# Kernel optimization log

Measured on AMD Instinct MI355X. Metric: run time of the kernel, lower is better.

Reference implementation:

```python
import jax, jax.numpy as jnp
import numpy as np

ITER_NUM = 3
BN_EPS = 1e-5
L2_EPS = 1e-12


def setup_inputs() -> dict:
    key = jax.random.key(0)
    k1, k2 = jax.random.split(key, 2)
    B, C, h, w = 64, 256, 14, 14
    E = 512
    feat = jax.random.normal(k1, (B, C, h, w), dtype=jnp.float32)
    W_proj = jax.random.normal(k2, (E, C * C), dtype=jnp.float32) * (1.0 / np.sqrt(C * C))
    b_proj = jnp.zeros((E,), dtype=jnp.float32)
    bn_gamma = jnp.ones((E,), dtype=jnp.float32)
    bn_beta = jnp.zeros((E,), dtype=jnp.float32)
    bn_mean = jnp.zeros((E,), dtype=jnp.float32)
    bn_var = jnp.ones((E,), dtype=jnp.float32)
    return {"feat": feat, "W_proj": W_proj, "b_proj": b_proj,
            "bn_gamma": bn_gamma, "bn_beta": bn_beta,
            "bn_mean": bn_mean, "bn_var": bn_var}


def _mpncov(feat):
    # feat: [B, C, h, w] -> [B, C, C] matrix square root of normalized covariance
    B, C, h, w = feat.shape
    M = h * w
    x = feat.reshape(B, C, M)
    # I_hat = I - (1/M) * ones  (centering matrix)
    I_hat = jnp.eye(M, dtype=feat.dtype) - (1.0 / M) * jnp.ones((M, M), dtype=feat.dtype)
    # y = x @ I_hat @ x^T / M  -> [B, C, C]
    xc = jnp.einsum('bcm,mn->bcn', x, I_hat)
    y = jnp.einsum('bcm,bdm->bcd', xc, x) / M
    trY = jnp.trace(y, axis1=-2, axis2=-1)  # [B]
    y = y / trY[:, None, None]
    I = jnp.broadcast_to(jnp.eye(C, dtype=feat.dtype), (B, C, C))
    Y, Z = y, I
    for _ in range(ITER_NUM):
        ZY = jnp.einsum('bij,bjk->bik', Z, Y)
        T = 3.0 * I - ZY
        Y = 0.5 * jnp.einsum('bij,bjk->bik', Y, T)
        Z = 0.5 * jnp.einsum('bij,bjk->bik', T, Z)
    return Y * jnp.sqrt(trY)[:, None, None]


def _l2_normalize(x, axis=-1):
    n = jnp.sqrt(jnp.sum(x * x, axis=axis, keepdims=True))
    return x / jnp.maximum(n, L2_EPS)


def reference(feat, W_proj, b_proj, bn_gamma, bn_beta, bn_mean, bn_var):
    B = feat.shape[0]
    pooled = _mpncov(feat)                      # [B, C, C]
    flat = pooled.reshape(B, -1)                # [B, C*C]
    flat = _l2_normalize(flat, axis=1)
    # dropout in eval mode = identity
    emb = flat @ W_proj.T + b_proj              # [B, E]
    # BatchNorm1d (inference mode, running stats)
    emb = (emb - bn_mean) * jax.lax.rsqrt(bn_var + BN_EPS) * bn_gamma + bn_beta
    norm_embedding = _l2_normalize(emb, axis=1)
    return norm_embedding
```

## Files before the change

### kernel.cpp

```cpp
#include <hip/hip_runtime.h>
#include <hip/hip_bf16.h>

#define BATCH 64
#define CDIM  256
#define MHW   196
#define MP    224
#define EDIM  512
#define CC    65536
#define NTRI  10

typedef __attribute__((ext_vector_type(8))) short short8_t;
typedef __attribute__((ext_vector_type(4))) float f32x4;
typedef __attribute__((ext_vector_type(4))) unsigned int u32x4;

static __device__ __forceinline__ short f2bf(float f) {
    __hip_bfloat16 h = __float2bfloat16(f);
    return (short)__builtin_bit_cast(unsigned short, h);
}

struct MMOp {
    const __hip_bfloat16* A;
    const __hip_bfloat16* B;
    const __hip_bfloat16* D;
    __hip_bfloat16*       out;
    const float*          alpha_ptr;
    int                   alpha_mode;
    float                 alpha_c, beta, gamma;
    float*                nrm;
};

__global__ __launch_bounds__(256) void k_center(const float* __restrict__ feat,
                                                __hip_bfloat16* __restrict__ xcb,
                                                float* __restrict__ rowsq)
{
    const int row = blockIdx.x * 4 + (threadIdx.x >> 6);
    const int l = threadIdx.x & 63;
    const float* src = feat + (size_t)row * MHW;
    float v0 = src[l];
    float v1 = src[l + 64];
    float v2 = src[l + 128];
    float v3 = (l + 192 < MHW) ? src[l + 192] : 0.0f;
    float s = v0 + v1 + v2 + v3;
    #pragma unroll
    for (int o = 32; o >= 1; o >>= 1) s += __shfl_xor(s, o, 64);
    const float mean = s * (1.0f / MHW);
    v0 -= mean; v1 -= mean; v2 -= mean;
    v3 = (l + 192 < MHW) ? (v3 - mean) : 0.0f;
    float sq = v0*v0 + v1*v1 + v2*v2 + v3*v3;
    #pragma unroll
    for (int o = 32; o >= 1; o >>= 1) sq += __shfl_xor(sq, o, 64);
    if (l == 0) rowsq[row] = sq;
    __hip_bfloat16* dst = xcb + (size_t)row * MP;
    dst[l]       = __float2bfloat16(v0);
    dst[l + 64]  = __float2bfloat16(v1);
    dst[l + 128] = __float2bfloat16(v2);
    if (l + 192 < MP) dst[l + 192] = __float2bfloat16(v3);
}

template<int KT, bool NORM>
__global__ __launch_bounds__(256) void k_mm(MMOp op0, MMOp op1)
{
    const MMOp& op = (blockIdx.y == 0) ? op0 : op1;

    __shared__ __hip_bfloat16 As[64][72];
    __shared__ __hip_bfloat16 Bs[64][72];
    __shared__ float red[4];
    __shared__ float s_alpha;

    const int b = blockIdx.x / NTRI;
    const int t = blockIdx.x - b * NTRI;
    int ti, tj;
    if (t < 4)      { ti = 0; tj = t; }
    else if (t < 7) { ti = 1; tj = t - 3; }
    else if (t < 9) { ti = 2; tj = t - 5; }
    else            { ti = 3; tj = 3; }

    const int tid = threadIdx.x;
    const int wv = tid >> 6, l = tid & 63;
    const int wr = wv >> 1, wc = wv & 1;
    const int lr = l & 15,  lg = l >> 4;

    if (op.alpha_mode) {
        float v = op.alpha_ptr[b * 256 + tid];
        #pragma unroll
        for (int o = 32; o >= 1; o >>= 1) v += __shfl_xor(v, o, 64);
        if (l == 0) red[wv] = v;
        __syncthreads();
        if (tid == 0) s_alpha = op.alpha_c / (red[0] + red[1] + red[2] + red[3]);
    } else if (tid == 0) {
        s_alpha = op.alpha_c;
    }

    const __hip_bfloat16* Ab = op.A + (size_t)b * (CDIM * KT) + (size_t)ti * 64 * KT;
    const __hip_bfloat16* Bb = op.B + (size_t)b * (CDIM * KT) + (size_t)tj * 64 * KT;

    f32x4 acc[2][2];
    #pragma unroll
    for (int i = 0; i < 2; i++)
        #pragma unroll
        for (int j = 0; j < 2; j++)
            #pragma unroll
            for (int r = 0; r < 4; r++) acc[i][j][r] = 0.0f;

    #pragma unroll
    for (int k0 = 0; k0 < KT; k0 += 64) {
        const int kw   = (KT - k0 >= 64) ? 64 : (KT - k0);
        const int segs = kw >> 3;
        __syncthreads();
        for (int u = tid; u < 64 * segs; u += 256) {
            const int row = u / segs;
            const int seg = u - row * segs;
            *reinterpret_cast<u32x4*>(&As[row][seg * 8]) =
                *reinterpret_cast<const u32x4*>(Ab + (size_t)row * KT + k0 + seg * 8);
            *reinterpret_cast<u32x4*>(&Bs[row][seg * 8]) =
                *reinterpret_cast<const u32x4*>(Bb + (size_t)row * KT + k0 + seg * 8);
        }
        __syncthreads();
        const int nks = kw >> 5;
        for (int ks = 0; ks < nks; ks++) {
            short8_t af[2], bfr[2];
            #pragma unroll
            for (int i = 0; i < 2; i++)
                af[i] = *reinterpret_cast<const short8_t*>(&As[wr * 32 + i * 16 + lr][ks * 32 + lg * 8]);
            #pragma unroll
            for (int j = 0; j < 2; j++)
                bfr[j] = *reinterpret_cast<const short8_t*>(&Bs[wc * 32 + j * 16 + lr][ks * 32 + lg * 8]);
            #pragma unroll
            for (int i = 0; i < 2; i++)
                #pragma unroll
                for (int j = 0; j < 2; j++)
                    acc[i][j] = __builtin_amdgcn_mfma_f32_16x16x32_bf16(af[i], bfr[j], acc[i][j], 0, 0, 0);
        }
    }

    const float a = s_alpha;
    __hip_bfloat16* ob = op.out + (size_t)b * CC;
    const __hip_bfloat16* Db = op.D ? (op.D + (size_t)b * CC) : nullptr;
    float ns = 0.0f;
    #pragma unroll
    for (int i = 0; i < 2; i++) {
        #pragma unroll
        for (int j = 0; j < 2; j++) {
            #pragma unroll
            for (int r = 0; r < 4; r++) {
                const int grow = ti * 64 + wr * 32 + i * 16 + lg * 4 + r;
                const int gcol = tj * 64 + wc * 32 + j * 16 + lr;
                float v = a * acc[i][j][r];
                if (Db) v += op.beta * __bfloat162float(Db[grow * 256 + gcol]);
                if (grow == gcol) v += op.gamma;
                const __hip_bfloat16 hv = __float2bfloat16(v);
                ob[grow * 256 + gcol] = hv;
                if (ti != tj) ob[gcol * 256 + grow] = hv;
                if (NORM) {
                    const float fv = __bfloat162float(hv);
                    ns += ((ti != tj) ? 2.0f : 1.0f) * fv * fv;
                }
            }
        }
    }
    if constexpr (NORM) {
        #pragma unroll
        for (int o = 32; o >= 1; o >>= 1) ns += __shfl_xor(ns, o, 64);
        __syncthreads();
        if (l == 0) red[wv] = ns;
        __syncthreads();
        if (tid == 0) op.nrm[b * NTRI + t] = red[0] + red[1] + red[2] + red[3];
    }
}

__global__ __launch_bounds__(256) void k_proj(const __hip_bfloat16* __restrict__ flat,
                                              const float* __restrict__ W,
                                              float* __restrict__ upart)
{
    const int ks = blockIdx.x;
    const int et = blockIdx.y;
    const int tid = threadIdx.x, wv = tid >> 6, l = tid & 63;
    const int lr = l & 15, lg = l >> 4;
    const int kbase = ks * 2048 + wv * 512;

    f32x4 acc[4][4];
    #pragma unroll
    for (int i = 0; i < 4; i++)
        #pragma unroll
        for (int j = 0; j < 4; j++)
            #pragma unroll
            for (int r = 0; r < 4; r++) acc[i][j][r] = 0.0f;

    for (int kk = 0; kk < 512; kk += 32) {
        const int k = kbase + kk + lg * 8;
        short8_t af[4];
        #pragma unroll
        for (int i = 0; i < 4; i++)
            af[i] = *reinterpret_cast<const short8_t*>(flat + (size_t)(i * 16 + lr) * CC + k);
        short8_t bfr[4];
        #pragma unroll
        for (int j = 0; j < 4; j++) {
            const f32x4* wp = reinterpret_cast<const f32x4*>(W + (size_t)(et * 64 + j * 16 + lr) * CC + k);
            const f32x4 w0 = wp[0], w1 = wp[1];
            short8_t s;
            s[0] = f2bf(w0[0]); s[1] = f2bf(w0[1]); s[2] = f2bf(w0[2]); s[3] = f2bf(w0[3]);
            s[4] = f2bf(w1[0]); s[5] = f2bf(w1[1]); s[6] = f2bf(w1[2]); s[7] = f2bf(w1[3]);
            bfr[j] = s;
        }
        #pragma unroll
        for (int i = 0; i < 4; i++)
            #pragma unroll
            for (int j = 0; j < 4; j++)
                acc[i][j] = __builtin_amdgcn_mfma_f32_16x16x32_bf16(af[i], bfr[j], acc[i][j], 0, 0, 0);
    }

    __shared__ float racc[2][64][65];
    if (wv >= 2) {
        #pragma unroll
        for (int i = 0; i < 4; i++)
            #pragma unroll
            for (int j = 0; j < 4; j++)
                #pragma unroll
                for (int r = 0; r < 4; r++)
                    racc[wv - 2][i * 16 + lg * 4 + r][j * 16 + lr] = acc[i][j][r];
    }
    __syncthreads();
    if (wv < 2) {
        #pragma unroll
        for (int i = 0; i < 4; i++)
            #pragma unroll
            for (int j = 0; j < 4; j++)
                #pragma unroll
                for (int r = 0; r < 4; r++)
                    racc[wv][i * 16 + lg * 4 + r][j * 16 + lr] += acc[i][j][r];
    }
    __syncthreads();
    float* ub = upart + (size_t)ks * (64 * EDIM);
    #pragma unroll
    for (int q = 0; q < 16; q++) {
        const int idx = q * 256 + tid;
        const int x = idx >> 6, y = idx & 63;
        ub[(size_t)x * EDIM + et * 64 + y] = racc[0][x][y] + racc[1][x][y];
    }
}

__global__ __launch_bounds__(512) void k_final(const float* __restrict__ upart,
                                               const float* __restrict__ nrmp,
                                               const float* __restrict__ bias,
                                               const float* __restrict__ gma,
                                               const float* __restrict__ bta,
                                               const float* __restrict__ mu,
                                               const float* __restrict__ var,
                                               float* __restrict__ out)
{
    const int b = blockIdx.x;
    const int e = threadIdx.x;
    float u = 0.0f;
    for (int p = 0; p < 32; p++)
        u += upart[((size_t)p * 64 + b) * EDIM + e];
    float fro = 0.0f;
    #pragma unroll
    for (int q = 0; q < NTRI; q++) fro += nrmp[b * NTRI + q];
    const float s = 1.0f / fmaxf(sqrtf(fro), 1e-12f);
    const float emb = s * u + bias[e];
    const float v = (emb - mu[e]) * rsqrtf(var[e] + 1e-5f) * gma[e] + bta[e];
    float sq = v * v;
    #pragma unroll
    for (int o = 32; o >= 1; o >>= 1) sq += __shfl_xor(sq, o, 64);
    __shared__ float wsum[8];
    if ((e & 63) == 0) wsum[e >> 6] = sq;
    __syncthreads();
    float tot = 0.0f;
    #pragma unroll
    for (int i = 0; i < 8; i++) tot += wsum[i];
    out[(size_t)b * EDIM + e] = v / fmaxf(sqrtf(tot), 1e-12f);
}

extern "C" void kernel_launch(void* const* d_in, const int* in_sizes, int n_in,
                              void* d_out, int out_size, void* d_ws, size_t ws_size,
                              hipStream_t stream)
{
    const float* feat = (const float*)d_in[0];
    const float* W    = (const float*)d_in[1];
    const float* bias = (const float*)d_in[2];
    const float* gma  = (const float*)d_in[3];
    const float* bta  = (const float*)d_in[4];
    const float* mu   = (const float*)d_in[5];
    const float* var  = (const float*)d_in[6];
    float* out = (float*)d_out;

    char* ws = (char*)d_ws;
    constexpr size_t XCB_BYTES = (size_t)BATCH * CDIM * MP * 2;
    constexpr size_t MATB      = (size_t)BATCH * CC * 2;
    constexpr size_t OFF_ROWSQ = 4096;
    constexpr size_t OFF_XCB   = OFF_ROWSQ + (size_t)BATCH * CDIM * 4;
    constexpr size_t OFF_M     = OFF_XCB + XCB_BYTES;
    constexpr size_t OFF_UP    = OFF_M + 5 * MATB;
    constexpr size_t NEEDED    = OFF_UP + (size_t)32 * 64 * EDIM * 4;
    if (ws_size < NEEDED) return;

    float* nrmp  = (float*)(ws + 1024);
    float* rowsq = (float*)(ws + OFF_ROWSQ);
    __hip_bfloat16* xcb = (__hip_bfloat16*)(ws + OFF_XCB);
    __hip_bfloat16* M0  = (__hip_bfloat16*)(ws + OFF_M + 0 * MATB);
    __hip_bfloat16* M1  = (__hip_bfloat16*)(ws + OFF_M + 1 * MATB);
    __hip_bfloat16* M2  = (__hip_bfloat16*)(ws + OFF_M + 2 * MATB);
    __hip_bfloat16* M3  = (__hip_bfloat16*)(ws + OFF_M + 3 * MATB);
    __hip_bfloat16* M4  = (__hip_bfloat16*)(ws + OFF_M + 4 * MATB);
    float* upart = (float*)(ws + OFF_UP);

    k_center<<<dim3(4096), dim3(256), 0, stream>>>(feat, xcb, rowsq);

    const dim3 g1(BATCH * NTRI, 1), g2(BATCH * NTRI, 2), blk(256);
    MMOp nop = {};

    MMOp cov = {xcb, xcb, nullptr, M0, rowsq, 1, 1.0f, 0.0f, 0.0f, nullptr};
    k_mm<MP, false><<<g1, blk, 0, stream>>>(cov, nop);
    MMOp y1 = {M0, M0, M0, M1, nullptr, 0, -0.5f, 1.5f, 0.0f, nullptr};
    k_mm<256, false><<<g1, blk, 0, stream>>>(y1, nop);
    MMOp t2 = {M0, M1, M1, M2, nullptr, 0, 0.5f, -1.5f, 3.0f, nullptr};
    k_mm<256, false><<<g1, blk, 0, stream>>>(t2, nop);
    MMOp y2 = {M1, M2, nullptr, M3, nullptr, 0, 0.5f, 0.0f, 0.0f, nullptr};
    MMOp z2 = {M2, M0, M2, M4, nullptr, 0, -0.25f, 0.75f, 0.0f, nullptr};
    k_mm<256, false><<<g2, blk, 0, stream>>>(y2, z2);
    MMOp t3 = {M4, M3, nullptr, M1, nullptr, 0, -1.0f, 0.0f, 3.0f, nullptr};
    k_mm<256, false><<<g1, blk, 0, stream>>>(t3, nop);
    MMOp y3 = {M3, M1, nullptr, M2, nullptr, 0, 0.5f, 0.0f, 0.0f, nrmp};
    k_mm<256, true ><<<g1, blk, 0, stream>>>(y3, nop);

    k_proj<<<dim3(32, 8), blk, 0, stream>>>(M2, W, upart);
    k_final<<<dim3(64), 512, 0, stream>>>(upart, nrmp, bias, gma, bta, mu, var, out);
}
```

Baseline: 133.1 us.

## Fuse Newton-Schulz chain into cooperative persistent kernel with grid syncs

Replaces the sequence of centering and batched matmul launches with one cooperative kernel that uses grid-wide syncs between stages. The projection and final normalization are fused into a second cooperative kernel. The projection K-split is doubled to give 512 blocks. This targets per-launch overhead and tail gaps between small dependent kernels. In exchange it adds grid.sync costs and host-side occupancy queries on every call, and it keeps a multi-launch fallback path.

```diff
diff --git a/kernel.cpp b/kernel.cpp
--- a/kernel.cpp
+++ b/kernel.cpp
@@ -1,5 +1,8 @@
 #include <hip/hip_runtime.h>
 #include <hip/hip_bf16.h>
+#include <hip/hip_cooperative_groups.h>
+
+namespace cg = cooperative_groups;
 
 #define BATCH 64
 #define CDIM  256
@@ -29,12 +32,10 @@
     float*                nrm;
 };
 
-__global__ __launch_bounds__(256) void k_center(const float* __restrict__ feat,
-                                                __hip_bfloat16* __restrict__ xcb,
-                                                float* __restrict__ rowsq)
-{
-    const int row = blockIdx.x * 4 + (threadIdx.x >> 6);
-    const int l = threadIdx.x & 63;
+static __device__ __forceinline__ void center_row(
+    const float* __restrict__ feat, __hip_bfloat16* __restrict__ xcb,
+    float* __restrict__ rowsq, int row, int l)
+{
     const float* src = feat + (size_t)row * MHW;
     float v0 = src[l];
     float v1 = src[l + 64];
@@ -58,17 +59,15 @@
 }
 
 template<int KT, bool NORM>
-__global__ __launch_bounds__(256) void k_mm(MMOp op0, MMOp op1)
-{
-    const MMOp& op = (blockIdx.y == 0) ? op0 : op1;
-
-    __shared__ __hip_bfloat16 As[64][72];
-    __shared__ __hip_bfloat16 Bs[64][72];
-    __shared__ float red[4];
-    __shared__ float s_alpha;
-
-    const int b = blockIdx.x / NTRI;
-    const int t = blockIdx.x - b * NTRI;
+static __device__ __forceinline__ void mm_tile(
+    const __hip_bfloat16* __restrict__ A, const __hip_bfloat16* __restrict__ Bm,
+    const __hip_bfloat16* __restrict__ D, __hip_bfloat16* __restrict__ out,
+    const float* __restrict__ alpha_ptr, int alpha_mode,
+    float alpha_c, float beta, float gamma, float* __restrict__ nrm,
+    int b, int t,
+    __hip_bfloat16 (*As)[72], __hip_bfloat16 (*Bs)[72],
+    float* red, float* s_alpha)
+{
     int ti, tj;
     if (t < 4)      { ti = 0; tj = t; }
     else if (t < 7) { ti = 1; tj = t - 3; }
@@ -80,19 +79,20 @@
     const int wr = wv >> 1, wc = wv & 1;
     const int lr = l & 15,  lg = l >> 4;
 
-    if (op.alpha_mode) {
-        float v = op.alpha_ptr[b * 256 + tid];
+    __syncthreads();
+    if (alpha_mode) {
+        float v = alpha_ptr[b * 256 + tid];
         #pragma unroll
         for (int o = 32; o >= 1; o >>= 1) v += __shfl_xor(v, o, 64);
         if (l == 0) red[wv] = v;
         __syncthreads();
-        if (tid == 0) s_alpha = op.alpha_c / (red[0] + red[1] + red[2] + red[3]);
+        if (tid == 0) *s_alpha = alpha_c / (red[0] + red[1] + red[2] + red[3]);
     } else if (tid == 0) {
-        s_alpha = op.alpha_c;
-    }
-
-    const __hip_bfloat16* Ab = op.A + (size_t)b * (CDIM * KT) + (size_t)ti * 64 * KT;
-    const __hip_bfloat16* Bb = op.B + (size_t)b * (CDIM * KT) + (size_t)tj * 64 * KT;
+        *s_alpha = alpha_c;
+    }
+
+    const __hip_bfloat16* Ab = A  + (size_t)b * (CDIM * KT) + (size_t)ti * 64 * KT;
+    const __hip_bfloat16* Bb = Bm + (size_t)b * (CDIM * KT) + (size_t)tj * 64 * KT;
 
     f32x4 acc[2][2];
     #pragma unroll
@@ -133,9 +133,9 @@
         }
     }
 
-    const float a = s_alpha;
-    __hip_bfloat16* ob = op.out + (size_t)b * CC;
-    const __hip_bfloat16* Db = op.D ? (op.D + (size_t)b * CC) : nullptr;
+    const float a = *s_alpha;
+    __hip_bfloat16* ob = out + (size_t)b * CC;
+    const __hip_bfloat16* Db = D ? (D + (size_t)b * CC) : nullptr;
     float ns = 0.0f;
     #pragma unroll
     for (int i = 0; i < 2; i++) {
@@ -146,8 +146,8 @@
                 const int grow = ti * 64 + wr * 32 + i * 16 + lg * 4 + r;
                 const int gcol = tj * 64 + wc * 32 + j * 16 + lr;
                 float v = a * acc[i][j][r];
-                if (Db) v += op.beta * __bfloat162float(Db[grow * 256 + gcol]);
-                if (grow == gcol) v += op.gamma;
+                if (Db) v += beta * __bfloat162float(Db[grow * 256 + gcol]);
+                if (grow == gcol) v += gamma;
                 const __hip_bfloat16 hv = __float2bfloat16(v);
                 ob[grow * 256 + gcol] = hv;
                 if (ti != tj) ob[gcol * 256 + grow] = hv;
@@ -164,19 +164,17 @@
         __syncthreads();
         if (l == 0) red[wv] = ns;
         __syncthreads();
-        if (tid == 0) op.nrm[b * NTRI + t] = red[0] + red[1] + red[2] + red[3];
-    }
-}
-
-__global__ __launch_bounds__(256) void k_proj(const __hip_bfloat16* __restrict__ flat,
-                                              const float* __restrict__ W,
-                                              float* __restrict__ upart)
-{
-    const int ks = blockIdx.x;
-    const int et = blockIdx.y;
+        if (tid == 0) nrm[b * NTRI + t] = red[0] + red[1] + red[2] + red[3];
+    }
+}
+
+static __device__ __forceinline__ void proj_body(
+    const __hip_bfloat16* __restrict__ flat, const float* __restrict__ W,
+    float* __restrict__ upart, int ks, int et, float (*racc)[64][65])
+{
     const int tid = threadIdx.x, wv = tid >> 6, l = tid & 63;
     const int lr = l & 15, lg = l >> 4;
-    const int kbase = ks * 2048 + wv * 512;
+    const int kbase = ks * 1024 + wv * 256;
 
     f32x4 acc[4][4];
     #pragma unroll
@@ -186,7 +184,7 @@
             #pragma unroll
             for (int r = 0; r < 4; r++) acc[i][j][r] = 0.0f;
 
-    for (int kk = 0; kk < 512; kk += 32) {
+    for (int kk = 0; kk < 256; kk += 32) {
         const int k = kbase + kk + lg * 8;
         short8_t af[4];
         #pragma unroll
@@ -209,7 +207,6 @@
                 acc[i][j] = __builtin_amdgcn_mfma_f32_16x16x32_bf16(af[i], bfr[j], acc[i][j], 0, 0, 0);
     }
 
-    __shared__ float racc[2][64][65];
     if (wv >= 2) {
         #pragma unroll
         for (int i = 0; i < 4; i++)
@@ -239,7 +236,123 @@
     }
 }
 
-__global__ __launch_bounds__(512) void k_final(const float* __restrict__ upart,
+static __device__ __forceinline__ void fin_body(
+    const float* __restrict__ upart, const float* __restrict__ nrmp,
+    const float* __restrict__ bias, const float* __restrict__ gma,
+    const float* __restrict__ bta, const float* __restrict__ mu,
+    const float* __restrict__ var, float* __restrict__ out, int bb, float* wsum)
+{
+    const int tid = threadIdx.x, wv = tid >> 6, l = tid & 63;
+    const int e0 = tid, e1 = tid + 256;
+    float u0 = 0.0f, u1 = 0.0f;
+    for (int p = 0; p < 64; ++p) {
+        const float* up = upart + ((size_t)p * 64 + bb) * EDIM;
+        u0 += up[e0]; u1 += up[e1];
+    }
+    float fro = 0.0f;
+    #pragma unroll
+    for (int q = 0; q < NTRI; ++q) fro += nrmp[bb * NTRI + q];
+    const float s = 1.0f / fmaxf(sqrtf(fro), 1e-12f);
+    const float emb0 = s * u0 + bias[e0];
+    const float emb1 = s * u1 + bias[e1];
+    const float v0 = (emb0 - mu[e0]) * rsqrtf(var[e0] + 1e-5f) * gma[e0] + bta[e0];
+    const float v1 = (emb1 - mu[e1]) * rsqrtf(var[e1] + 1e-5f) * gma[e1] + bta[e1];
+    float sq = v0 * v0 + v1 * v1;
+    #pragma unroll
+    for (int o = 32; o >= 1; o >>= 1) sq += __shfl_xor(sq, o, 64);
+    if (l == 0) wsum[wv] = sq;
+    __syncthreads();
+    const float tot = wsum[0] + wsum[1] + wsum[2] + wsum[3];
+    const float rn = 1.0f / fmaxf(sqrtf(tot), 1e-12f);
+    out[(size_t)bb * EDIM + e0] = v0 * rn;
+    out[(size_t)bb * EDIM + e1] = v1 * rn;
+}
+
+__global__ __launch_bounds__(256, 4) void k_ns_coop(
+    const float* __restrict__ feat, __hip_bfloat16* __restrict__ xcb,
+    float* __restrict__ rowsq,
+    __hip_bfloat16* __restrict__ M0, __hip_bfloat16* __restrict__ M1,
+    __hip_bfloat16* __restrict__ M2, __hip_bfloat16* __restrict__ M3,
+    __hip_bfloat16* __restrict__ M4, float* __restrict__ nrmp)
+{
+    cg::grid_group grid = cg::this_grid();
+    __shared__ __hip_bfloat16 As[64][72];
+    __shared__ __hip_bfloat16 Bs[64][72];
+    __shared__ float red[4];
+    __shared__ float s_alpha;
+
+    const int tid = threadIdx.x, wv = tid >> 6, l = tid & 63;
+
+    #pragma unroll
+    for (int it = 0; it < 7; ++it) {
+        const int row = it * 2560 + blockIdx.x * 4 + wv;
+        if (row < BATCH * CDIM) center_row(feat, xcb, rowsq, row, l);
+    }
+    __threadfence(); grid.sync();
+
+    const int b = blockIdx.x / NTRI;
+    const int t = blockIdx.x - b * NTRI;
+
+    mm_tile<MP, false>(xcb, xcb, nullptr, M0, rowsq, 1, 1.0f, 0.0f, 0.0f, nullptr, b, t, As, Bs, red, &s_alpha);
+    __threadfence(); grid.sync();
+    mm_tile<256, false>(M0, M0, M0, M1, nullptr, 0, -0.5f, 1.5f, 0.0f, nullptr, b, t, As, Bs, red, &s_alpha);
+    __threadfence(); grid.sync();
+    mm_tile<256, false>(M0, M1, M1, M2, nullptr, 0, 0.5f, -1.5f, 3.0f, nullptr, b, t, As, Bs, red, &s_alpha);
+    __threadfence(); grid.sync();
+    mm_tile<256, false>(M1, M2, nullptr, M3, nullptr, 0, 0.5f, 0.0f, 0.0f, nullptr, b, t, As, Bs, red, &s_alpha);
+    mm_tile<256, false>(M2, M0, M2, M4, nullptr, 0, -0.25f, 0.75f, 0.0f, nullptr, b, t, As, Bs, red, &s_alpha);
+    __threadfence(); grid.sync();
+    mm_tile<256, false>(M4, M3, nullptr, M1, nullptr, 0, -1.0f, 0.0f, 3.0f, nullptr, b, t, As, Bs, red, &s_alpha);
+    __threadfence(); grid.sync();
+    mm_tile<256, true>(M3, M1, nullptr, M2, nullptr, 0, 0.5f, 0.0f, 0.0f, nrmp, b, t, As, Bs, red, &s_alpha);
+}
+
+__global__ __launch_bounds__(256, 2) void k_pf_coop(
+    const __hip_bfloat16* __restrict__ flat, const float* __restrict__ W,
+    float* __restrict__ upart, const float* __restrict__ nrmp,
+    const float* __restrict__ bias, const float* __restrict__ gma,
+    const float* __restrict__ bta, const float* __restrict__ mu,
+    const float* __restrict__ var, float* __restrict__ out)
+{
+    cg::grid_group grid = cg::this_grid();
+    __shared__ float racc[2][64][65];
+    __shared__ float wsum[4];
+    proj_body(flat, W, upart, blockIdx.x >> 3, blockIdx.x & 7, racc);
+    __threadfence(); grid.sync();
+    if (blockIdx.x < BATCH)
+        fin_body(upart, nrmp, bias, gma, bta, mu, var, out, blockIdx.x, wsum);
+}
+
+__global__ __launch_bounds__(256) void k_center_f(const float* __restrict__ feat,
+                                                  __hip_bfloat16* __restrict__ xcb,
+                                                  float* __restrict__ rowsq)
+{
+    center_row(feat, xcb, rowsq, blockIdx.x * 4 + (threadIdx.x >> 6), threadIdx.x & 63);
+}
+
+template<int KT, bool NORM>
+__global__ __launch_bounds__(256) void k_mm_f(MMOp op0, MMOp op1)
+{
+    const MMOp op = (blockIdx.y == 0) ? op0 : op1;
+    __shared__ __hip_bfloat16 As[64][72];
+    __shared__ __hip_bfloat16 Bs[64][72];
+    __shared__ float red[4];
+    __shared__ float s_alpha;
+    const int b = blockIdx.x / NTRI;
+    const int t = blockIdx.x - b * NTRI;
+    mm_tile<KT, NORM>(op.A, op.B, op.D, op.out, op.alpha_ptr, op.alpha_mode,
+                      op.alpha_c, op.beta, op.gamma, op.nrm, b, t, As, Bs, red, &s_alpha);
+}
+
+__global__ __launch_bounds__(256) void k_proj_f(const __hip_bfloat16* __restrict__ flat,
+                                                const float* __restrict__ W,
+                                                float* __restrict__ upart)
+{
+    __shared__ float racc[2][64][65];
+    proj_body(flat, W, upart, blockIdx.x, blockIdx.y, racc);
+}
+
+__global__ __launch_bounds__(256) void k_fin_f(const float* __restrict__ upart,
                                                const float* __restrict__ nrmp,
                                                const float* __restrict__ bias,
                                                const float* __restrict__ gma,
@@ -248,27 +361,8 @@
                                                const float* __restrict__ var,
                                                float* __restrict__ out)
 {
-    const int b = blockIdx.x;
-    const int e = threadIdx.x;
-    float u = 0.0f;
-    for (int p = 0; p < 32; p++)
-        u += upart[((size_t)p * 64 + b) * EDIM + e];
-    float fro = 0.0f;
-    #pragma unroll
-    for (int q = 0; q < NTRI; q++) fro += nrmp[b * NTRI + q];
-    const float s = 1.0f / fmaxf(sqrtf(fro), 1e-12f);
-    const float emb = s * u + bias[e];
-    const float v = (emb - mu[e]) * rsqrtf(var[e] + 1e-5f) * gma[e] + bta[e];
-    float sq = v * v;
-    #pragma unroll
-    for (int o = 32; o >= 1; o >>= 1) sq += __shfl_xor(sq, o, 64);
-    __shared__ float wsum[8];
-    if ((e & 63) == 0) wsum[e >> 6] = sq;
-    __syncthreads();
-    float tot = 0.0f;
-    #pragma unroll
-    for (int i = 0; i < 8; i++) tot += wsum[i];
-    out[(size_t)b * EDIM + e] = v / fmaxf(sqrtf(tot), 1e-12f);
+    __shared__ float wsum[4];
+    fin_body(upart, nrmp, bias, gma, bta, mu, var, out, blockIdx.x, wsum);
 }
 
 extern "C" void kernel_launch(void* const* d_in, const int* in_sizes, int n_in,
@@ -291,7 +385,7 @@
     constexpr size_t OFF_XCB   = OFF_ROWSQ + (size_t)BATCH * CDIM * 4;
     constexpr size_t OFF_M     = OFF_XCB + XCB_BYTES;
     constexpr size_t OFF_UP    = OFF_M + 5 * MATB;
-    constexpr size_t NEEDED    = OFF_UP + (size_t)32 * 64 * EDIM * 4;
+    constexpr size_t NEEDED    = OFF_UP + (size_t)64 * 64 * EDIM * 4;
     if (ws_size < NEEDED) return;
 
     float* nrmp  = (float*)(ws + 1024);
@@ -304,25 +398,58 @@
     __hip_bfloat16* M4  = (__hip_bfloat16*)(ws + OFF_M + 4 * MATB);
     float* upart = (float*)(ws + OFF_UP);
 
-    k_center<<<dim3(4096), dim3(256), 0, stream>>>(feat, xcb, rowsq);
-
-    const dim3 g1(BATCH * NTRI, 1), g2(BATCH * NTRI, 2), blk(256);
-    MMOp nop = {};
-
-    MMOp cov = {xcb, xcb, nullptr, M0, rowsq, 1, 1.0f, 0.0f, 0.0f, nullptr};
-    k_mm<MP, false><<<g1, blk, 0, stream>>>(cov, nop);
-    MMOp y1 = {M0, M0, M0, M1, nullptr, 0, -0.5f, 1.5f, 0.0f, nullptr};
-    k_mm<256, false><<<g1, blk, 0, stream>>>(y1, nop);
-    MMOp t2 = {M0, M1, M1, M2, nullptr, 0, 0.5f, -1.5f, 3.0f, nullptr};
-    k_mm<256, false><<<g1, blk, 0, stream>>>(t2, nop);
-    MMOp y2 = {M1, M2, nullptr, M3, nullptr, 0, 0.5f, 0.0f, 0.0f, nullptr};
-    MMOp z2 = {M2, M0, M2, M4, nullptr, 0, -0.25f, 0.75f, 0.0f, nullptr};
-    k_mm<256, false><<<g2, blk, 0, stream>>>(y2, z2);
-    MMOp t3 = {M4, M3, nullptr, M1, nullptr, 0, -1.0f, 0.0f, 3.0f, nullptr};
-    k_mm<256, false><<<g1, blk, 0, stream>>>(t3, nop);
-    MMOp y3 = {M3, M1, nullptr, M2, nullptr, 0, 0.5f, 0.0f, 0.0f, nrmp};
-    k_mm<256, true ><<<g1, blk, 0, stream>>>(y3, nop);
-
-    k_proj<<<dim3(32, 8), blk, 0, stream>>>(M2, W, upart);
-    k_final<<<dim3(64), 512, 0, stream>>>(upart, nrmp, bias, gma, bta, mu, var, out);
-}
+    int dev = 0; hipGetDevice(&dev);
+    int coop = 0, ncu = 0;
+    hipDeviceGetAttribute(&coop, hipDeviceAttributeCooperativeLaunch, dev);
+    hipDeviceGetAttribute(&ncu, hipDeviceAttributeMultiprocessorCount, dev);
+    int mb_ns = 0, mb_pf = 0;
+    hipOccupancyMaxActiveBlocksPerMultiprocessor(&mb_ns, (const void*)k_ns_coop, 256, 0);
+    hipOccupancyMaxActiveBlocksPerMultiprocessor(&mb_pf, (const void*)k_pf_coop, 256, 0);
+    bool use_coop = (coop != 0) && ((long)mb_ns * ncu >= BATCH * NTRI)
+                                && ((long)mb_pf * ncu >= 512);
+
+    bool coop_done = false;
+    if (use_coop) {
+        void* argsA[] = {(void*)&feat, (void*)&xcb, (void*)&rowsq,
+                         (void*)&M0, (void*)&M1, (void*)&M2, (void*)&M3, (void*)&M4,
+                         (void*)&nrmp};
+        hipError_t eA = hipLaunchCooperativeKernel((void*)k_ns_coop,
+                            dim3(BATCH * NTRI), dim3(256), argsA, 0, stream);
+        if (eA == hipSuccess) {
+            const __hip_bfloat16* flat = M2;
+            void* argsB[] = {(void*)&flat, (void*)&W, (void*)&upart, (void*)&nrmp,
+                             (void*)&bias, (void*)&gma, (void*)&bta, (void*)&mu,
+                             (void*)&var, (void*)&out};
+            hipError_t eB = hipLaunchCooperativeKernel((void*)k_pf_coop,
+                                dim3(512), dim3(256), argsB, 0, stream);
+            if (eB == hipSuccess) {
+                coop_done = true;
+            } else {
+                k_proj_f<<<dim3(64, 8), 256, 0, stream>>>(M2, W, upart);
+                k_fin_f<<<dim3(64), 256, 0, stream>>>(upart, nrmp, bias, gma, bta, mu, var, out);
+                coop_done = true;
+            }
+        }
+    }
+
+    if (!coop_done) {
+        k_center_f<<<dim3(4096), 256, 0, stream>>>(feat, xcb, rowsq);
+        const dim3 g1(BATCH * NTRI, 1), g2(BATCH * NTRI, 2), blk(256);
+        MMOp nop = {};
+        MMOp cov = {xcb, xcb, nullptr, M0, rowsq, 1, 1.0f, 0.0f, 0.0f, nullptr};
+        k_mm_f<MP, false><<<g1, blk, 0, stream>>>(cov, nop);
+        MMOp y1 = {M0, M0, M0, M1, nullptr, 0, -0.5f, 1.5f, 0.0f, nullptr};
+        k_mm_f<256, false><<<g1, blk, 0, stream>>>(y1, nop);
+        MMOp t2 = {M0, M1, M1, M2, nullptr, 0, 0.5f, -1.5f, 3.0f, nullptr};
+        k_mm_f<256, false><<<g1, blk, 0, stream>>>(t2, nop);
+        MMOp y2 = {M1, M2, nullptr, M3, nullptr, 0, 0.5f, 0.0f, 0.0f, nullptr};
+        MMOp z2 = {M2, M0, M2, M4, nullptr, 0, -0.25f, 0.75f, 0.0f, nullptr};
+        k_mm_f<256, false><<<g2, blk, 0, stream>>>(y2, z2);
+        MMOp t3 = {M4, M3, nullptr, M1, nullptr, 0, -1.0f, 0.0f, 3.0f, nullptr};
+        k_mm_f<256, false><<<g1, blk, 0, stream>>>(t3, nop);
+        MMOp y3 = {M3, M1, nullptr, M2, nullptr, 0, 0.5f, 0.0f, 0.0f, nrmp};
+        k_mm_f<256, true ><<<g1, blk, 0, stream>>>(y3, nop);
+        k_proj_f<<<dim3(64, 8), 256, 0, stream>>>(M2, W, upart);
+        k_fin_f<<<dim3(64), 256, 0, stream>>>(upart, nrmp, bias, gma, bta, mu, var, out);
+    }
+}
```

Measured after the change: 133.8 us. Within noise of the previous version (+0.5%).

## Overlap W fp32-to-bf16 conversion with covariance kernels via extra blocks

Applied to the files above, without the earlier changes.

The fp32 projection weight is converted to bf16 by extra blocks appended to the centering and matmul launches, spreading the conversion across the otherwise underfilled kernels. The projection kernel then reads pre-converted bf16 weights with twice as many K-splits (64x8 grid), and the final kernel sums 64 partials. This aims to hide the large W read behind the small batched matmuls and to halve the weight bytes the projection streams, at the cost of extra workspace and a write plus re-read of the bf16 copy.

```diff
diff --git a/kernel.cpp b/kernel.cpp
--- a/kernel.cpp
+++ b/kernel.cpp
@@ -8,14 +8,16 @@
 #define EDIM  512
 #define CC    65536
 #define NTRI  10
+#define NMM   (BATCH * NTRI)
+#define NCONV_TOTAL 2048
 
 typedef __attribute__((ext_vector_type(8))) short short8_t;
 typedef __attribute__((ext_vector_type(4))) float f32x4;
 typedef __attribute__((ext_vector_type(4))) unsigned int u32x4;
 
-static __device__ __forceinline__ short f2bf(float f) {
+static __device__ __forceinline__ unsigned short f2bfu(float f) {
     __hip_bfloat16 h = __float2bfloat16(f);
-    return (short)__builtin_bit_cast(unsigned short, h);
+    return __builtin_bit_cast(unsigned short, h);
 }
 
 struct MMOp {
@@ -29,10 +31,30 @@
     float*                nrm;
 };
 
+static __device__ __forceinline__ void conv_w(const float* __restrict__ W,
+                                              __hip_bfloat16* __restrict__ Wbf,
+                                              int cb, int it0, int it1, int tid)
+{
+    const size_t base = (size_t)cb * 4096;
+    for (int it = it0; it < it1; ++it) {
+        const size_t idx = (base + (size_t)it * 256 + tid) * 4;
+        const f32x4 v = *reinterpret_cast<const f32x4*>(W + idx);
+        ushort4 o;
+        o.x = f2bfu(v[0]); o.y = f2bfu(v[1]); o.z = f2bfu(v[2]); o.w = f2bfu(v[3]);
+        *reinterpret_cast<ushort4*>(Wbf + idx) = o;
+    }
+}
+
 __global__ __launch_bounds__(256) void k_center(const float* __restrict__ feat,
                                                 __hip_bfloat16* __restrict__ xcb,
-                                                float* __restrict__ rowsq)
-{
+                                                float* __restrict__ rowsq,
+                                                const float* __restrict__ W,
+                                                __hip_bfloat16* __restrict__ Wbf)
+{
+    if (blockIdx.x >= 4096) {
+        conv_w(W, Wbf, blockIdx.x - 4096, 0, 16, threadIdx.x);
+        return;
+    }
     const int row = blockIdx.x * 4 + (threadIdx.x >> 6);
     const int l = threadIdx.x & 63;
     const float* src = feat + (size_t)row * MHW;
@@ -58,9 +80,20 @@
 }
 
 template<int KT, bool NORM>
-__global__ __launch_bounds__(256) void k_mm(MMOp op0, MMOp op1)
-{
-    const MMOp& op = (blockIdx.y == 0) ? op0 : op1;
+__global__ __launch_bounds__(256) void k_mm(MMOp op0, MMOp op1,
+                                            const float* __restrict__ W,
+                                            __hip_bfloat16* __restrict__ Wbf,
+                                            int conv_base)
+{
+    const int tid = threadIdx.x;
+    if (blockIdx.x >= NMM) {
+        const int cb = conv_base + (blockIdx.x - NMM);
+        if (gridDim.y == 2) conv_w(W, Wbf, cb, blockIdx.y * 8, blockIdx.y * 8 + 8, tid);
+        else                conv_w(W, Wbf, cb, 0, 16, tid);
+        return;
+    }
+
+    const MMOp op = (blockIdx.y == 0) ? op0 : op1;
 
     __shared__ __hip_bfloat16 As[64][72];
     __shared__ __hip_bfloat16 Bs[64][72];
@@ -75,7 +108,6 @@
     else if (t < 9) { ti = 2; tj = t - 5; }
     else            { ti = 3; tj = 3; }
 
-    const int tid = threadIdx.x;
     const int wv = tid >> 6, l = tid & 63;
     const int wr = wv >> 1, wc = wv & 1;
     const int lr = l & 15,  lg = l >> 4;
@@ -168,15 +200,15 @@
     }
 }
 
-__global__ __launch_bounds__(256) void k_proj(const __hip_bfloat16* __restrict__ flat,
-                                              const float* __restrict__ W,
-                                              float* __restrict__ upart)
-{
-    const int ks = blockIdx.x;
-    const int et = blockIdx.y;
+__global__ __launch_bounds__(256) void k_proj2(const __hip_bfloat16* __restrict__ flat,
+                                               const __hip_bfloat16* __restrict__ Wbf,
+                                               float* __restrict__ upart)
+{
+    __shared__ float racc[2][64][65];
+    const int ks = blockIdx.x, et = blockIdx.y;
     const int tid = threadIdx.x, wv = tid >> 6, l = tid & 63;
     const int lr = l & 15, lg = l >> 4;
-    const int kbase = ks * 2048 + wv * 512;
+    const int kbase = ks * 1024 + wv * 256;
 
     f32x4 acc[4][4];
     #pragma unroll
@@ -186,22 +218,15 @@
             #pragma unroll
             for (int r = 0; r < 4; r++) acc[i][j][r] = 0.0f;
 
-    for (int kk = 0; kk < 512; kk += 32) {
+    for (int kk = 0; kk < 256; kk += 32) {
         const int k = kbase + kk + lg * 8;
-        short8_t af[4];
+        short8_t af[4], bfr[4];
         #pragma unroll
         for (int i = 0; i < 4; i++)
             af[i] = *reinterpret_cast<const short8_t*>(flat + (size_t)(i * 16 + lr) * CC + k);
-        short8_t bfr[4];
-        #pragma unroll
-        for (int j = 0; j < 4; j++) {
-            const f32x4* wp = reinterpret_cast<const f32x4*>(W + (size_t)(et * 64 + j * 16 + lr) * CC + k);
-            const f32x4 w0 = wp[0], w1 = wp[1];
-            short8_t s;
-            s[0] = f2bf(w0[0]); s[1] = f2bf(w0[1]); s[2] = f2bf(w0[2]); s[3] = f2bf(w0[3]);
-            s[4] = f2bf(w1[0]); s[5] = f2bf(w1[1]); s[6] = f2bf(w1[2]); s[7] = f2bf(w1[3]);
-            bfr[j] = s;
-        }
+        #pragma unroll
+        for (int j = 0; j < 4; j++)
+            bfr[j] = *reinterpret_cast<const short8_t*>(Wbf + (size_t)(et * 64 + j * 16 + lr) * CC + k);
         #pragma unroll
         for (int i = 0; i < 4; i++)
             #pragma unroll
@@ -209,7 +234,6 @@
                 acc[i][j] = __builtin_amdgcn_mfma_f32_16x16x32_bf16(af[i], bfr[j], acc[i][j], 0, 0, 0);
     }
 
-    __shared__ float racc[2][64][65];
     if (wv >= 2) {
         #pragma unroll
         for (int i = 0; i < 4; i++)
@@ -239,36 +263,41 @@
     }
 }
 
-__global__ __launch_bounds__(512) void k_final(const float* __restrict__ upart,
-                                               const float* __restrict__ nrmp,
-                                               const float* __restrict__ bias,
-                                               const float* __restrict__ gma,
-                                               const float* __restrict__ bta,
-                                               const float* __restrict__ mu,
-                                               const float* __restrict__ var,
-                                               float* __restrict__ out)
-{
-    const int b = blockIdx.x;
-    const int e = threadIdx.x;
-    float u = 0.0f;
-    for (int p = 0; p < 32; p++)
-        u += upart[((size_t)p * 64 + b) * EDIM + e];
+__global__ __launch_bounds__(256) void k_fin(const float* __restrict__ upart,
+                                             const float* __restrict__ nrmp,
+                                             const float* __restrict__ bias,
+                                             const float* __restrict__ gma,
+                                             const float* __restrict__ bta,
+                                             const float* __restrict__ mu,
+                                             const float* __restrict__ var,
+                                             float* __restrict__ out)
+{
+    __shared__ float wsum[4];
+    const int bb = blockIdx.x;
+    const int tid = threadIdx.x, wv = tid >> 6, l = tid & 63;
+    const int e0 = tid, e1 = tid + 256;
+    float u0 = 0.0f, u1 = 0.0f;
+    for (int p = 0; p < 64; ++p) {
+        const float* up = upart + ((size_t)p * 64 + bb) * EDIM;
+        u0 += up[e0]; u1 += up[e1];
+    }
     float fro = 0.0f;
     #pragma unroll
-    for (int q = 0; q < NTRI; q++) fro += nrmp[b * NTRI + q];
+    for (int q = 0; q < NTRI; ++q) fro += nrmp[bb * NTRI + q];
     const float s = 1.0f / fmaxf(sqrtf(fro), 1e-12f);
-    const float emb = s * u + bias[e];
-    const float v = (emb - mu[e]) * rsqrtf(var[e] + 1e-5f) * gma[e] + bta[e];
-    float sq = v * v;
+    const float emb0 = s * u0 + bias[e0];
+    const float emb1 = s * u1 + bias[e1];
+    const float v0 = (emb0 - mu[e0]) * rsqrtf(var[e0] + 1e-5f) * gma[e0] + bta[e0];
+    const float v1 = (emb1 - mu[e1]) * rsqrtf(var[e1] + 1e-5f) * gma[e1] + bta[e1];
+    float sq = v0 * v0 + v1 * v1;
     #pragma unroll
     for (int o = 32; o >= 1; o >>= 1) sq += __shfl_xor(sq, o, 64);
-    __shared__ float wsum[8];
-    if ((e & 63) == 0) wsum[e >> 6] = sq;
+    if (l == 0) wsum[wv] = sq;
     __syncthreads();
-    float tot = 0.0f;
-    #pragma unroll
-    for (int i = 0; i < 8; i++) tot += wsum[i];
-    out[(size_t)b * EDIM + e] = v / fmaxf(sqrtf(tot), 1e-12f);
+    const float tot = wsum[0] + wsum[1] + wsum[2] + wsum[3];
+    const float rn = 1.0f / fmaxf(sqrtf(tot), 1e-12f);
+    out[(size_t)bb * EDIM + e0] = v0 * rn;
+    out[(size_t)bb * EDIM + e1] = v1 * rn;
 }
 
 extern "C" void kernel_launch(void* const* d_in, const int* in_sizes, int n_in,
@@ -287,11 +316,13 @@
     char* ws = (char*)d_ws;
     constexpr size_t XCB_BYTES = (size_t)BATCH * CDIM * MP * 2;
     constexpr size_t MATB      = (size_t)BATCH * CC * 2;
+    constexpr size_t WBF_BYTES = (size_t)CC * EDIM * 2;
     constexpr size_t OFF_ROWSQ = 4096;
     constexpr size_t OFF_XCB   = OFF_ROWSQ + (size_t)BATCH * CDIM * 4;
     constexpr size_t OFF_M     = OFF_XCB + XCB_BYTES;
-    constexpr size_t OFF_UP    = OFF_M + 5 * MATB;
-    constexpr size_t NEEDED    = OFF_UP + (size_t)32 * 64 * EDIM * 4;
+    constexpr size_t OFF_WBF   = OFF_M + 5 * MATB;
+    constexpr size_t OFF_UP    = OFF_WBF + WBF_BYTES;
+    constexpr size_t NEEDED    = OFF_UP + (size_t)64 * 64 * EDIM * 4;
     if (ws_size < NEEDED) return;
 
     float* nrmp  = (float*)(ws + 1024);
@@ -302,27 +333,28 @@
     __hip_bfloat16* M2  = (__hip_bfloat16*)(ws + OFF_M + 2 * MATB);
     __hip_bfloat16* M3  = (__hip_bfloat16*)(ws + OFF_M + 3 * MATB);
     __hip_bfloat16* M4  = (__hip_bfloat16*)(ws + OFF_M + 4 * MATB);
+    __hip_bfloat16* Wbf = (__hip_bfloat16*)(ws + OFF_WBF);
     float* upart = (float*)(ws + OFF_UP);
 
-    k_center<<<dim3(4096), dim3(256), 0, stream>>>(feat, xcb, rowsq);
-
-    const dim3 g1(BATCH * NTRI, 1), g2(BATCH * NTRI, 2), blk(256);
+    k_center<<<dim3(4096 + 296), 256, 0, stream>>>(feat, xcb, rowsq, W, Wbf);
+
+    const dim3 g1(NMM + 292, 1), g2(NMM + 292, 2), blk(256);
     MMOp nop = {};
 
     MMOp cov = {xcb, xcb, nullptr, M0, rowsq, 1, 1.0f, 0.0f, 0.0f, nullptr};
-    k_mm<MP, false><<<g1, blk, 0, stream>>>(cov, nop);
+    k_mm<MP, false><<<g1, blk, 0, stream>>>(cov, nop, W, Wbf, 296);
     MMOp y1 = {M0, M0, M0, M1, nullptr, 0, -0.5f, 1.5f, 0.0f, nullptr};
-    k_mm<256, false><<<g1, blk, 0, stream>>>(y1, nop);
+    k_mm<256, false><<<g1, blk, 0, stream>>>(y1, nop, W, Wbf, 588);
     MMOp t2 = {M0, M1, M1, M2, nullptr, 0, 0.5f, -1.5f, 3.0f, nullptr};
-    k_mm<256, false><<<g1, blk, 0, stream>>>(t2, nop);
+    k_mm<256, false><<<g1, blk, 0, stream>>>(t2, nop, W, Wbf, 880);
     MMOp y2 = {M1, M2, nullptr, M3, nullptr, 0, 0.5f, 0.0f, 0.0f, nullptr};
     MMOp z2 = {M2, M0, M2, M4, nullptr, 0, -0.25f, 0.75f, 0.0f, nullptr};
-    k_mm<256, false><<<g2, blk, 0, stream>>>(y2, z2);
+    k_mm<256, false><<<g2, blk, 0, stream>>>(y2, z2, W, Wbf, 1172);
     MMOp t3 = {M4, M3, nullptr, M1, nullptr, 0, -1.0f, 0.0f, 3.0f, nullptr};
-    k_mm<256, false><<<g1, blk, 0, stream>>>(t3, nop);
+    k_mm<256, false><<<g1, blk, 0, stream>>>(t3, nop, W, Wbf, 1464);
     MMOp y3 = {M3, M1, nullptr, M2, nullptr, 0, 0.5f, 0.0f, 0.0f, nrmp};
-    k_mm<256, true ><<<g1, blk, 0, stream>>>(y3, nop);
-
-    k_proj<<<dim3(32, 8), blk, 0, stream>>>(M2, W, upart);
-    k_final<<<dim3(64), 512, 0, stream>>>(upart, nrmp, bias, gma, bta, mu, var, out);
-}
+    k_mm<256, true ><<<g1, blk, 0, stream>>>(y3, nop, W, Wbf, 1756);
+
+    k_proj2<<<dim3(64, 8), blk, 0, stream>>>(M2, Wbf, upart);
+    k_fin<<<dim3(64), blk, 0, stream>>>(upart, nrmp, bias, gma, bta, mu, var, out);
+}
```

Measured after the change: 157.8 us. +18.5%, slower.

## Double split-K blocks in projection and remap block indices batch-minor

Applied to the files above, without the earlier changes.

The projection GEMM now uses 64 K-splits of 1024 instead of 32 of 2048, doubling the grid to 512 blocks to spread the large fp32 weight stream over more CUs. The final reduction kernel sums 64 partials with 256 threads each handling two outputs. Block indexing in k_center and k_mm is remapped so consecutive blocks walk across batches rather than within one batch, changing how work is spread over CUs and the cache. The trade-off is twice the partial-sum workspace traffic and a longer reduction in the final kernel.

```diff
diff --git a/kernel.cpp b/kernel.cpp
--- a/kernel.cpp
+++ b/kernel.cpp
@@ -8,6 +8,7 @@
 #define EDIM  512
 #define CC    65536
 #define NTRI  10
+#define NMM   (BATCH * NTRI)
 
 typedef __attribute__((ext_vector_type(8))) short short8_t;
 typedef __attribute__((ext_vector_type(4))) float f32x4;
@@ -33,7 +34,9 @@
                                                 __hip_bfloat16* __restrict__ xcb,
                                                 float* __restrict__ rowsq)
 {
-    const int row = blockIdx.x * 4 + (threadIdx.x >> 6);
+    const int b  = blockIdx.x & 63;
+    const int r4 = blockIdx.x >> 6;
+    const int row = b * 256 + r4 * 4 + (threadIdx.x >> 6);
     const int l = threadIdx.x & 63;
     const float* src = feat + (size_t)row * MHW;
     float v0 = src[l];
@@ -60,15 +63,15 @@
 template<int KT, bool NORM>
 __global__ __launch_bounds__(256) void k_mm(MMOp op0, MMOp op1)
 {
-    const MMOp& op = (blockIdx.y == 0) ? op0 : op1;
+    const MMOp op = (blockIdx.y == 0) ? op0 : op1;
 
     __shared__ __hip_bfloat16 As[64][72];
     __shared__ __hip_bfloat16 Bs[64][72];
     __shared__ float red[4];
     __shared__ float s_alpha;
 
-    const int b = blockIdx.x / NTRI;
-    const int t = blockIdx.x - b * NTRI;
+    const int b = blockIdx.x & 63;
+    const int t = blockIdx.x >> 6;
     int ti, tj;
     if (t < 4)      { ti = 0; tj = t; }
     else if (t < 7) { ti = 1; tj = t - 3; }
@@ -172,11 +175,11 @@
                                               const float* __restrict__ W,
                                               float* __restrict__ upart)
 {
-    const int ks = blockIdx.x;
-    const int et = blockIdx.y;
+    __shared__ float racc[2][64][65];
+    const int ks = blockIdx.x, et = blockIdx.y;
     const int tid = threadIdx.x, wv = tid >> 6, l = tid & 63;
     const int lr = l & 15, lg = l >> 4;
-    const int kbase = ks * 2048 + wv * 512;
+    const int kbase = ks * 1024 + wv * 256;
 
     f32x4 acc[4][4];
     #pragma unroll
@@ -186,7 +189,7 @@
             #pragma unroll
             for (int r = 0; r < 4; r++) acc[i][j][r] = 0.0f;
 
-    for (int kk = 0; kk < 512; kk += 32) {
+    for (int kk = 0; kk < 256; kk += 32) {
         const int k = kbase + kk + lg * 8;
         short8_t af[4];
         #pragma unroll
@@ -209,7 +212,6 @@
                 acc[i][j] = __builtin_amdgcn_mfma_f32_16x16x32_bf16(af[i], bfr[j], acc[i][j], 0, 0, 0);
     }
 
-    __shared__ float racc[2][64][65];
     if (wv >= 2) {
         #pragma unroll
         for (int i = 0; i < 4; i++)
@@ -239,36 +241,41 @@
     }
 }
 
-__global__ __launch_bounds__(512) void k_final(const float* __restrict__ upart,
-                                               const float* __restrict__ nrmp,
-                                               const float* __restrict__ bias,
-                                               const float* __restrict__ gma,
-                                               const float* __restrict__ bta,
-                                               const float* __restrict__ mu,
-                                               const float* __restrict__ var,
-                                               float* __restrict__ out)
-{
-    const int b = blockIdx.x;
-    const int e = threadIdx.x;
-    float u = 0.0f;
-    for (int p = 0; p < 32; p++)
-        u += upart[((size_t)p * 64 + b) * EDIM + e];
+__global__ __launch_bounds__(256) void k_fin(const float* __restrict__ upart,
+                                             const float* __restrict__ nrmp,
+                                             const float* __restrict__ bias,
+                                             const float* __restrict__ gma,
+                                             const float* __restrict__ bta,
+                                             const float* __restrict__ mu,
+                                             const float* __restrict__ var,
+                                             float* __restrict__ out)
+{
+    __shared__ float wsum[4];
+    const int bb = blockIdx.x;
+    const int tid = threadIdx.x, wv = tid >> 6, l = tid & 63;
+    const int e0 = tid, e1 = tid + 256;
+    float u0 = 0.0f, u1 = 0.0f;
+    for (int p = 0; p < 64; ++p) {
+        const float* up = upart + ((size_t)p * 64 + bb) * EDIM;
+        u0 += up[e0]; u1 += up[e1];
+    }
     float fro = 0.0f;
     #pragma unroll
-    for (int q = 0; q < NTRI; q++) fro += nrmp[b * NTRI + q];
+    for (int q = 0; q < NTRI; ++q) fro += nrmp[bb * NTRI + q];
     const float s = 1.0f / fmaxf(sqrtf(fro), 1e-12f);
-    const float emb = s * u + bias[e];
-    const float v = (emb - mu[e]) * rsqrtf(var[e] + 1e-5f) * gma[e] + bta[e];
-    float sq = v * v;
+    const float emb0 = s * u0 + bias[e0];
+    const float emb1 = s * u1 + bias[e1];
+    const float v0 = (emb0 - mu[e0]) * rsqrtf(var[e0] + 1e-5f) * gma[e0] + bta[e0];
+    const float v1 = (emb1 - mu[e1]) * rsqrtf(var[e1] + 1e-5f) * gma[e1] + bta[e1];
+    float sq = v0 * v0 + v1 * v1;
     #pragma unroll
     for (int o = 32; o >= 1; o >>= 1) sq += __shfl_xor(sq, o, 64);
-    __shared__ float wsum[8];
-    if ((e & 63) == 0) wsum[e >> 6] = sq;
+    if (l == 0) wsum[wv] = sq;
     __syncthreads();
-    float tot = 0.0f;
-    #pragma unroll
-    for (int i = 0; i < 8; i++) tot += wsum[i];
-    out[(size_t)b * EDIM + e] = v / fmaxf(sqrtf(tot), 1e-12f);
+    const float tot = wsum[0] + wsum[1] + wsum[2] + wsum[3];
+    const float rn = 1.0f / fmaxf(sqrtf(tot), 1e-12f);
+    out[(size_t)bb * EDIM + e0] = v0 * rn;
+    out[(size_t)bb * EDIM + e1] = v1 * rn;
 }
 
 extern "C" void kernel_launch(void* const* d_in, const int* in_sizes, int n_in,
@@ -291,7 +298,7 @@
     constexpr size_t OFF_XCB   = OFF_ROWSQ + (size_t)BATCH * CDIM * 4;
     constexpr size_t OFF_M     = OFF_XCB + XCB_BYTES;
     constexpr size_t OFF_UP    = OFF_M + 5 * MATB;
-    constexpr size_t NEEDED    = OFF_UP + (size_t)32 * 64 * EDIM * 4;
+    constexpr size_t NEEDED    = OFF_UP + (size_t)64 * 64 * EDIM * 4;
     if (ws_size < NEEDED) return;
 
     float* nrmp  = (float*)(ws + 1024);
@@ -304,9 +311,9 @@
     __hip_bfloat16* M4  = (__hip_bfloat16*)(ws + OFF_M + 4 * MATB);
     float* upart = (float*)(ws + OFF_UP);
 
-    k_center<<<dim3(4096), dim3(256), 0, stream>>>(feat, xcb, rowsq);
-
-    const dim3 g1(BATCH * NTRI, 1), g2(BATCH * NTRI, 2), blk(256);
+    k_center<<<dim3(4096), 256, 0, stream>>>(feat, xcb, rowsq);
+
+    const dim3 g1(NMM, 1), g2(NMM, 2), blk(256);
     MMOp nop = {};
 
     MMOp cov = {xcb, xcb, nullptr, M0, rowsq, 1, 1.0f, 0.0f, 0.0f, nullptr};
@@ -323,6 +330,6 @@
     MMOp y3 = {M3, M1, nullptr, M2, nullptr, 0, 0.5f, 0.0f, 0.0f, nrmp};
     k_mm<256, true ><<<g1, blk, 0, stream>>>(y3, nop);
 
-    k_proj<<<dim3(32, 8), blk, 0, stream>>>(M2, W, upart);
-    k_final<<<dim3(64), 512, 0, stream>>>(upart, nrmp, bias, gma, bta, mu, var, out);
-}
+    k_proj<<<dim3(64, 8), blk, 0, stream>>>(M2, W, upart);
+    k_fin<<<dim3(64), blk, 0, stream>>>(upart, nrmp, bias, gma, bta, mu, var, out);
+}
```

Result: faster. 115.1 us (median of 2 runs) (-13.6%).
